# Kernel optimization log

Hardware: AMD Instinct MI355X
Metric: run time of the kernel (lower is better)

The kernel has to match this reference:

```python
import jax, jax.numpy as jnp
import numpy as np

INPUT_SIZE = 64


def _xavier(key, shape):
    fan_in, fan_out = shape[1], shape[0]
    bound = float(np.sqrt(6.0 / (fan_in + fan_out)))
    return jax.random.uniform(key, shape, jnp.float32, -bound, bound)


def setup_inputs() -> dict:
    key = jax.random.key(0)
    k_x, k_wih, k_whh, k_wout = jax.random.split(key, 4)
    B, N, F = 32768, 16, INPUT_SIZE + 1
    inputs = jax.random.normal(k_x, (B, N, F), jnp.float32)
    # GRU(input_size, hidden=1): weight_ih [3*1, input_size], weight_hh [3*1, 1]
    W_ih = _xavier(k_wih, (3, INPUT_SIZE))
    W_hh = _xavier(k_whh, (3, 1))
    b_ih = jnp.zeros((3,), jnp.float32)
    b_hh = jnp.zeros((3,), jnp.float32)
    # Linear(1, 1)
    w_out = _xavier(k_wout, (1, 1))
    b_out = jnp.zeros((1,), jnp.float32)
    return {"inputs": inputs, "W_ih": W_ih, "W_hh": W_hh, "b_ih": b_ih,
            "b_hh": b_hh, "w_out": w_out, "b_out": b_out}


def reference(inputs, W_ih, W_hh, b_ih, b_hh, w_out, b_out):
    B, N, F = inputs.shape
    x = inputs[..., 1:].reshape(B * N, F - 1)   # GRU input, one timestep
    h = inputs[..., :1].reshape(B * N, 1)       # initial hidden state
    # Single GRU cell step (PyTorch gate ordering: r, z, n)
    gi = x @ W_ih.T + b_ih                      # [BN, 3]
    gh = h @ W_hh.T + b_hh                      # [BN, 3]
    r = jax.nn.sigmoid(gi[:, 0:1] + gh[:, 0:1])
    z = jax.nn.sigmoid(gi[:, 1:2] + gh[:, 1:2])
    n = jnp.tanh(gi[:, 2:3] + r * gh[:, 2:3])
    h_new = (1.0 - z) * n + z * h               # [BN, 1]
    out = h_new * w_out[0, 0] + b_out[0]        # Linear(1,1)
    return out.reshape(B, N, 1)
```

## Files before the change

### kernel.cpp

```cpp
#include <hip/hip_runtime.h>
#include <math.h>


#define THREADS 128
#define RPB 32
#define ROW_F 65
#define REGION_F (RPB * ROW_F)
#define REGION_B (REGION_F * 4)
#define FULL_ITERS 4
#define TAIL_F4 8

__device__ __forceinline__ float sigmoidf_(float v) {
    return 1.0f / (1.0f + __expf(-v));
}

__device__ __forceinline__ void async_copy16(const void* g, void* l) {
    __builtin_amdgcn_global_load_lds(
        (const __attribute__((address_space(1))) void*)g,
        (__attribute__((address_space(3))) void*)l,
        16, 0, 0);
}

__global__ __launch_bounds__(THREADS)
void gru_cell_kernel(const float* __restrict__ inputs,
                     const float* __restrict__ W_ih,
                     const float* __restrict__ W_hh,
                     const float* __restrict__ b_ih,
                     const float* __restrict__ b_hh,
                     const float* __restrict__ w_out,
                     const float* __restrict__ b_out,
                     float* __restrict__ out)
{
    __shared__ float ldsRow[REGION_F];
    __shared__ float ldsW[192];

    const int tid  = threadIdx.x;
    const size_t base = (size_t)blockIdx.x * REGION_F;
    const char* gsrc = (const char*)(inputs + base);

    const int wave_off = (tid >> 6) << 10;
    #pragma unroll
    for (int it = 0; it < FULL_ITERS; ++it) {
        async_copy16(gsrc + it * 2048 + tid * 16,
                     (char*)ldsRow + it * 2048 + wave_off);
    }
    if (tid < TAIL_F4) {
        reinterpret_cast<float4*>(ldsRow)[FULL_ITERS * 128 + tid] =
            reinterpret_cast<const float4*>(gsrc)[FULL_ITERS * 128 + tid];
    }
    if (tid < 48) {
        reinterpret_cast<float4*>(ldsW)[tid] =
            reinterpret_cast<const float4*>(W_ih)[tid];
    }

    __syncthreads();

    const int r = tid >> 2;
    const int q = tid & 3;
    const float* x  = ldsRow + r * ROW_F + 1 + q * 16;
    const float* w0 = ldsW +   0 + q * 16;
    const float* w1 = ldsW +  64 + q * 16;
    const float* w2 = ldsW + 128 + q * 16;

    float a0 = 0.0f, a1 = 0.0f, a2 = 0.0f;
    #pragma unroll
    for (int j = 0; j < 16; ++j) {
        const float xv = x[j];
        a0 = fmaf(xv, w0[j], a0);
        a1 = fmaf(xv, w1[j], a1);
        a2 = fmaf(xv, w2[j], a2);
    }

    a0 += __shfl_xor(a0, 1); a0 += __shfl_xor(a0, 2);
    a1 += __shfl_xor(a1, 1); a1 += __shfl_xor(a1, 2);
    a2 += __shfl_xor(a2, 1); a2 += __shfl_xor(a2, 2);

    const float h = ldsRow[r * ROW_F];
    const float gh0 = fmaf(h, W_hh[0], b_hh[0]);
    const float gh1 = fmaf(h, W_hh[1], b_hh[1]);
    const float gh2 = fmaf(h, W_hh[2], b_hh[2]);

    const float rg = sigmoidf_(a0 + b_ih[0] + gh0);
    const float zg = sigmoidf_(a1 + b_ih[1] + gh1);
    const float ng = tanhf(a2 + b_ih[2] + rg * gh2);
    const float h_new = (1.0f - zg) * ng + zg * h;

    if (q == 0) {
        out[(size_t)blockIdx.x * RPB + r] = fmaf(h_new, w_out[0], b_out[0]);
    }
}

extern "C" void kernel_launch(void* const* d_in, const int* in_sizes, int n_in,
                              void* d_out, int out_size, void* d_ws, size_t ws_size,
                              hipStream_t stream) {
    const float* inputs = (const float*)d_in[0];
    const float* W_ih   = (const float*)d_in[1];
    const float* W_hh   = (const float*)d_in[2];
    const float* b_ih   = (const float*)d_in[3];
    const float* b_hh   = (const float*)d_in[4];
    const float* w_out  = (const float*)d_in[5];
    const float* b_out  = (const float*)d_in[6];
    float* out = (float*)d_out;

    const int nrows  = in_sizes[0] / ROW_F;
    const int blocks = nrows / RPB;

    gru_cell_kernel<<<dim3(blocks), dim3(THREADS), 0, stream>>>(
        inputs, W_ih, W_hh, b_ih, b_hh, w_out, b_out, out);
}
```

Before: 26.21 us.

## Make blocks persistent with double-buffered async LDS staging of input regions

```diff
diff --git a/kernel.cpp b/kernel.cpp
--- a/kernel.cpp
+++ b/kernel.cpp
@@ -6,9 +6,8 @@
 #define RPB 32
 #define ROW_F 65
 #define REGION_F (RPB * ROW_F)
-#define REGION_B (REGION_F * 4)
 #define FULL_ITERS 4
-#define TAIL_F4 8
+#define NBLOCKS 2048
 
 __device__ __forceinline__ float sigmoidf_(float v) {
     return 1.0f / (1.0f + __expf(-v));
@@ -21,6 +20,21 @@
         16, 0, 0);
 }
 
+__device__ __forceinline__ void stage_region(const float* __restrict__ inputs,
+                                             size_t region, float* buf, int tid)
+{
+    const char* gsrc = (const char*)(inputs + region * REGION_F);
+    const int wave_off = (tid >> 6) << 10;
+    #pragma unroll
+    for (int it = 0; it < FULL_ITERS; ++it) {
+        async_copy16(gsrc + it * 2048 + tid * 16,
+                     (char*)buf + it * 2048 + wave_off);
+    }
+    if (tid < 8) {
+        async_copy16(gsrc + 8192 + tid * 16, (char*)buf + 8192);
+    }
+}
+
 __global__ __launch_bounds__(THREADS)
 void gru_cell_kernel(const float* __restrict__ inputs,
                      const float* __restrict__ W_ih,
@@ -29,64 +43,69 @@
                      const float* __restrict__ b_hh,
                      const float* __restrict__ w_out,
                      const float* __restrict__ b_out,
-                     float* __restrict__ out)
+                     float* __restrict__ out,
+                     int iters)
 {
-    __shared__ float ldsRow[REGION_F];
+    __shared__ float ldsRow[2][REGION_F];
     __shared__ float ldsW[192];
 
-    const int tid  = threadIdx.x;
-    const size_t base = (size_t)blockIdx.x * REGION_F;
-    const char* gsrc = (const char*)(inputs + base);
+    const int tid = threadIdx.x;
 
-    const int wave_off = (tid >> 6) << 10;
-    #pragma unroll
-    for (int it = 0; it < FULL_ITERS; ++it) {
-        async_copy16(gsrc + it * 2048 + tid * 16,
-                     (char*)ldsRow + it * 2048 + wave_off);
-    }
-    if (tid < TAIL_F4) {
-        reinterpret_cast<float4*>(ldsRow)[FULL_ITERS * 128 + tid] =
-            reinterpret_cast<const float4*>(gsrc)[FULL_ITERS * 128 + tid];
-    }
     if (tid < 48) {
         reinterpret_cast<float4*>(ldsW)[tid] =
             reinterpret_cast<const float4*>(W_ih)[tid];
     }
 
-    __syncthreads();
+    const size_t region0 = (size_t)blockIdx.x * iters;
+    stage_region(inputs, region0, ldsRow[0], tid);
 
     const int r = tid >> 2;
     const int q = tid & 3;
-    const float* x  = ldsRow + r * ROW_F + 1 + q * 16;
     const float* w0 = ldsW +   0 + q * 16;
     const float* w1 = ldsW +  64 + q * 16;
     const float* w2 = ldsW + 128 + q * 16;
 
-    float a0 = 0.0f, a1 = 0.0f, a2 = 0.0f;
-    #pragma unroll
-    for (int j = 0; j < 16; ++j) {
-        const float xv = x[j];
-        a0 = fmaf(xv, w0[j], a0);
-        a1 = fmaf(xv, w1[j], a1);
-        a2 = fmaf(xv, w2[j], a2);
-    }
+    const float Whh0 = W_hh[0], Whh1 = W_hh[1], Whh2 = W_hh[2];
+    const float bh0 = b_hh[0], bh1 = b_hh[1], bh2 = b_hh[2];
+    const float bi0 = b_ih[0], bi1 = b_ih[1], bi2 = b_ih[2];
+    const float wo = w_out[0], bo = b_out[0];
 
-    a0 += __shfl_xor(a0, 1); a0 += __shfl_xor(a0, 2);
-    a1 += __shfl_xor(a1, 1); a1 += __shfl_xor(a1, 2);
-    a2 += __shfl_xor(a2, 1); a2 += __shfl_xor(a2, 2);
+    for (int i = 0; i < iters; ++i) {
+        __syncthreads();
 
-    const float h = ldsRow[r * ROW_F];
-    const float gh0 = fmaf(h, W_hh[0], b_hh[0]);
-    const float gh1 = fmaf(h, W_hh[1], b_hh[1]);
-    const float gh2 = fmaf(h, W_hh[2], b_hh[2]);
+        if (i + 1 < iters) {
+            stage_region(inputs, region0 + i + 1, ldsRow[(i + 1) & 1], tid);
+        }
 
-    const float rg = sigmoidf_(a0 + b_ih[0] + gh0);
-    const float zg = sigmoidf_(a1 + b_ih[1] + gh1);
-    const float ng = tanhf(a2 + b_ih[2] + rg * gh2);
-    const float h_new = (1.0f - zg) * ng + zg * h;
+        const float* buf = ldsRow[i & 1];
+        const float* x = buf + r * ROW_F + 1 + q * 16;
 
-    if (q == 0) {
-        out[(size_t)blockIdx.x * RPB + r] = fmaf(h_new, w_out[0], b_out[0]);
+        float a0 = 0.0f, a1 = 0.0f, a2 = 0.0f;
+        #pragma unroll
+        for (int j = 0; j < 16; ++j) {
+            const float xv = x[j];
+            a0 = fmaf(xv, w0[j], a0);
+            a1 = fmaf(xv, w1[j], a1);
+            a2 = fmaf(xv, w2[j], a2);
+        }
+
+        a0 += __shfl_xor(a0, 1); a0 += __shfl_xor(a0, 2);
+        a1 += __shfl_xor(a1, 1); a1 += __shfl_xor(a1, 2);
+        a2 += __shfl_xor(a2, 1); a2 += __shfl_xor(a2, 2);
+
+        const float h = buf[r * ROW_F];
+        const float gh0 = fmaf(h, Whh0, bh0);
+        const float gh1 = fmaf(h, Whh1, bh1);
+        const float gh2 = fmaf(h, Whh2, bh2);
+
+        const float rg = sigmoidf_(a0 + bi0 + gh0);
+        const float zg = sigmoidf_(a1 + bi1 + gh1);
+        const float ng = tanhf(a2 + bi2 + rg * gh2);
+        const float h_new = (1.0f - zg) * ng + zg * h;
+
+        if (q == 0) {
+            out[(region0 + i) * RPB + r] = fmaf(h_new, wo, bo);
+        }
     }
 }
 
@@ -102,9 +121,10 @@
     const float* b_out  = (const float*)d_in[6];
     float* out = (float*)d_out;
 
-    const int nrows  = in_sizes[0] / ROW_F;
-    const int blocks = nrows / RPB;
+    const int nrows    = in_sizes[0] / ROW_F;
+    const int nregions = nrows / RPB;
+    const int iters    = nregions / NBLOCKS;
 
-    gru_cell_kernel<<<dim3(blocks), dim3(THREADS), 0, stream>>>(
-        inputs, W_ih, W_hh, b_ih, b_hh, w_out, b_out, out);
+    gru_cell_kernel<<<dim3(NBLOCKS), dim3(THREADS), 0, stream>>>(
+        inputs, W_ih, W_hh, b_ih, b_hh, w_out, b_out, out, iters);
 }
```

After: 26.37 us. Within noise of the previous version (+0.6%).
